# Performance work log

Measured on AMD Instinct MI355X. Metric: run time of the kernel, lower is better.

Reference implementation:

```python
import jax, jax.numpy as jnp
import numpy as np

N = 100000
E = 1600000
D = 128


def setup_inputs() -> dict:
    key = jax.random.key(0)
    k1, k2, k3 = jax.random.split(key, 3)
    indices = jax.random.randint(k1, (2, E), 0, N, dtype=jnp.int64)
    values = jax.random.normal(k2, (E,), dtype=jnp.float32)
    b = jax.random.normal(k3, (N, D), dtype=jnp.float32)
    return {"indices": indices, "values": values, "n": N, "b": b}


def reference(indices, values, n, b):
    # Sparse COO SpMM: out[r] = sum_{e: row[e]==r} values[e] * b[col[e]]
    row, col = indices[0], indices[1]
    contrib = values[:, None] * b[col]          # [E, D] gather-multiply
    out = jax.ops.segment_sum(contrib, row, num_segments=n)  # [N, D] scatter-add
    return out
```

## Files before the change

### kernel.cpp

```cpp
#include <hip/hip_runtime.h>
#include <hip/hip_fp16.h>


#define D_DIM 128
#define RPB 64
#define RPB_SHIFT 6
#define CRB 256
#define CRB_SHIFT 8
#define MAXCB 512
#define CCAP 4608
#define MAXB 2048
#define CAP_LDS 1408
#define EPT 6
#define EPT1 8
#define CHUNK1 4096
#define EPC 4
#define EPC2 5
#define OVF_T 8192

typedef float fx4 __attribute__((ext_vector_type(4)));

__global__ __launch_bounds__(256) void convert_b_kernel(
        const float* __restrict__ b, __half* __restrict__ bh, int n8) {
    int i = blockIdx.x * blockDim.x + threadIdx.x;
    if (i >= n8) return;
    const float4* b4 = (const float4*)b;
    float4 a0 = b4[2 * i];
    float4 a1 = b4[2 * i + 1];
    union { __half2 h[4]; uint4 u; } pk;
    pk.h[0] = __floats2half2_rn(a0.x, a0.y);
    pk.h[1] = __floats2half2_rn(a0.z, a0.w);
    pk.h[2] = __floats2half2_rn(a1.x, a1.y);
    pk.h[3] = __floats2half2_rn(a1.z, a1.w);
    ((uint4*)bh)[i] = pk.u;
}

__global__ __launch_bounds__(1024) void p1_sortcoarse(
        const int* __restrict__ rows,
        const int* __restrict__ cols,
        const float* __restrict__ vals,
        int* __restrict__ coarse_cnt,
        int2* __restrict__ coarse,
        int* __restrict__ ovf_cnt,
        int* __restrict__ ovf3,
        int E, int ncb, int ccap) {
    __shared__ int hist[MAXCB];
    __shared__ int cursor[MAXCB];
    __shared__ int2 stage[CHUNK1];
    __shared__ unsigned short sbkt[CHUNK1];

    int tid = threadIdx.x;
    int start = blockIdx.x * CHUNK1;
    int end = start + CHUNK1; if (end > E) end = E;
    int n = end - start;

    for (int i = tid; i < ncb; i += 1024) hist[i] = 0;
    __syncthreads();

    int rr[EPC]; int cc[EPC]; float vv[EPC];
    int ne = 0;
    for (int e = start + tid; e < end; e += 1024) {
        int r = rows[e];
        if (ne < EPC) { rr[ne] = r; cc[ne] = cols[e]; vv[ne] = vals[e]; }
        ++ne;
        atomicAdd(&hist[r >> CRB_SHIFT], 1);
    }
    __syncthreads();

    for (int d = 1; d < ncb; d <<= 1) {
        int t = (tid < ncb && tid >= d) ? hist[tid - d] : 0;
        __syncthreads();
        if (tid < ncb && tid >= d) hist[tid] += t;
        __syncthreads();
    }

    int incl = 0, excl = 0;
    if (tid < ncb) { incl = hist[tid]; excl = tid ? hist[tid - 1] : 0; }
    __syncthreads();
    if (tid < ncb) {
        int cnt = incl - excl;
        cursor[tid] = excl;
        int gres = (cnt > 0) ? atomicAdd(&coarse_cnt[tid], cnt) : 0;
        hist[tid] = gres - excl;
    }
    __syncthreads();

    for (int j = 0; j < ne; ++j) {
        int r, c; float v;
        if (j < EPC) { r = rr[j]; c = cc[j]; v = vv[j]; }
        else { int e = start + tid + j * 1024; r = rows[e]; c = cols[e]; v = vals[e]; }
        int bkt = r >> CRB_SHIFT;
        int pos = atomicAdd(&cursor[bkt], 1);
        stage[pos] = make_int2(((r & (CRB - 1)) << 17) | c, __float_as_int(v));
        sbkt[pos] = (unsigned short)bkt;
    }
    __syncthreads();

    for (int i = tid; i < n; i += 1024) {
        int bkt = sbkt[i];
        int2 e = stage[i];
        int gidx = i + hist[bkt];
        if (gidx < ccap) {
            coarse[(size_t)bkt * ccap + gidx] = e;
        } else {
            int k = atomicAdd(ovf_cnt, 1);
            if (k < OVF_T) {
                int r = (bkt << CRB_SHIFT) | ((unsigned)e.x >> 17);
                ovf3[3 * k] = r; ovf3[3 * k + 1] = e.x & 0x1FFFF;
                ovf3[3 * k + 2] = e.y;
            }
        }
    }
}

__global__ __launch_bounds__(1024) void p2_rowsort(
        const int* __restrict__ coarse_cnt,
        int2* __restrict__ coarse,
        int* __restrict__ row_beg,
        int* __restrict__ row_num,
        int ccap, int N) {
    __shared__ int2 stage[CCAP];
    __shared__ int hist[CRB];
    __shared__ int offs[CRB + 1];
    __shared__ int cursor[CRB];

    int bin = blockIdx.x;
    int tid = threadIdx.x;
    int cnt = coarse_cnt[bin];
    if (cnt > ccap) cnt = ccap;
    int2* cb = coarse + (size_t)bin * ccap;

    if (tid < CRB) hist[tid] = 0;
    __syncthreads();

    int2 ev[EPC2];
    int  rl[EPC2];
    int ne = 0;
    for (int i = tid; i < cnt; i += 1024) {
        int2 e = cb[i];
        ev[ne] = e;
        rl[ne] = ((unsigned)e.x) >> 17;
        atomicAdd(&hist[rl[ne]], 1);
        ++ne;
    }
    __syncthreads();

    for (int d = 1; d < CRB; d <<= 1) {
        int t = (tid < CRB && tid >= d) ? hist[tid - d] : 0;
        __syncthreads();
        if (tid < CRB) hist[tid] += (tid >= d) ? t : 0;
        __syncthreads();
    }
    if (tid == 0) offs[0] = 0;
    if (tid < CRB) {
        offs[tid + 1] = hist[tid];
        cursor[tid] = (tid == 0) ? 0 : hist[tid - 1];
    }
    __syncthreads();

    for (int j = 0; j < ne; ++j) {
        int pos = atomicAdd(&cursor[rl[j]], 1);
        stage[pos] = make_int2(ev[j].x & 0x1FFFF, ev[j].y);
    }
    __syncthreads();

    for (int i = tid; i < cnt; i += 1024) cb[i] = stage[i];
    if (tid < CRB) {
        int r = (bin << CRB_SHIFT) + tid;
        if (r < N) {
            row_beg[r] = bin * ccap + offs[tid];
            row_num[r] = offs[tid + 1] - offs[tid];
        }
    }
}

template <bool HALF>
__global__ __launch_bounds__(256) void csr_gather(
        const int* __restrict__ row_beg,
        const int* __restrict__ row_num,
        const int2* __restrict__ csr,
        const __half* __restrict__ bh,
        const float* __restrict__ b,
        float* __restrict__ out,
        int N) {
    int g = threadIdx.x >> 5;
    int glane = threadIdx.x & 31;
    int r = blockIdx.x * 8 + g;
    if (r >= N) return;

    int beg = row_beg[r];
    int num = row_num[r];
    const int2* pk = csr + beg;

    float4 acc = make_float4(0.f, 0.f, 0.f, 0.f);
    for (int base = 0; base < num; base += 8) {
#pragma unroll
        for (int j = 0; j < 8; ++j) {
            int idx = base + j;
            int sidx = (idx < num) ? idx : (num - 1);
            int2 e = pk[sidx];
            float v = (idx < num) ? __int_as_float(e.y) : 0.f;
            if (HALF) {
                uint2 hv = ((const uint2*)(bh + (size_t)e.x * D_DIM))[glane];
                __half2* hp = (__half2*)&hv;
                float2 f0 = __half22float2(hp[0]);
                float2 f1 = __half22float2(hp[1]);
                acc.x += v * f0.x;
                acc.y += v * f0.y;
                acc.z += v * f1.x;
                acc.w += v * f1.y;
            } else {
                float4 bv = ((const float4*)(b + (size_t)e.x * D_DIM))[glane];
                acc.x += v * bv.x;
                acc.y += v * bv.y;
                acc.z += v * bv.z;
                acc.w += v * bv.w;
            }
        }
    }
    fx4 av = {acc.x, acc.y, acc.z, acc.w};
    __builtin_nontemporal_store(av, (fx4*)(out + (size_t)r * D_DIM) + glane);
}


__global__ __launch_bounds__(1024) void phase1_partition(
        const int* __restrict__ rows,
        const int* __restrict__ cols,
        const float* __restrict__ vals,
        int* __restrict__ bucket_cnt,
        int2* __restrict__ packed,
        int* __restrict__ ovf_cnt,
        int* __restrict__ ovf3,
        int E, int nb, int cap, int chunk) {
    __shared__ int hist[MAXB];
    int tid = threadIdx.x;
    int start = blockIdx.x * chunk;
    int end = start + chunk; if (end > E) end = E;

    for (int i = tid; i < nb; i += 1024) hist[i] = 0;
    __syncthreads();

    int rr[EPT1]; int cc[EPT1]; float vv[EPT1];
    int ne = 0;
    for (int e = start + tid; e < end; e += 1024) {
        int r = rows[e];
        if (ne < EPT1) { rr[ne] = r; cc[ne] = cols[e]; vv[ne] = vals[e]; }
        ++ne;
        atomicAdd(&hist[r >> RPB_SHIFT], 1);
    }
    __syncthreads();

    for (int bkt = tid; bkt < nb; bkt += 1024) {
        int c = hist[bkt];
        hist[bkt] = (c > 0) ? atomicAdd(&bucket_cnt[bkt], c) : 0;
    }
    __syncthreads();

    int j = 0;
    for (int e = start + tid; e < end; e += 1024, ++j) {
        int r, c; float v;
        if (j < EPT1) { r = rr[j]; c = cc[j]; v = vv[j]; }
        else          { r = rows[e]; c = cols[e]; v = vals[e]; }
        int bkt = r >> RPB_SHIFT;
        int local = atomicAdd(&hist[bkt], 1);
        if (local < cap) {
            int key = ((r & (RPB - 1)) << 17) | c;
            packed[(size_t)bkt * cap + local] = make_int2(key, __float_as_int(v));
        } else {
            int k = atomicAdd(ovf_cnt, 1);
            if (k < OVF_T) {
                ovf3[3 * k] = r; ovf3[3 * k + 1] = c;
                ovf3[3 * k + 2] = __float_as_int(v);
            }
        }
    }
}

template <bool HALF>
__global__ __launch_bounds__(256) void phase2_sort_gather(
        const int* __restrict__ bucket_cnt,
        const int2* __restrict__ packed,
        const __half* __restrict__ bh,
        const float* __restrict__ b,
        float* __restrict__ out,
        int cap, int N) {
    __shared__ int2 sorted[CAP_LDS];
    __shared__ int hist[RPB];
    __shared__ int offs[RPB + 1];
    __shared__ int cursor[RPB];

    int bucket = blockIdx.x;
    int tid = threadIdx.x;

    int cnt = bucket_cnt[bucket];
    if (cnt > cap) cnt = cap;
    const int2* pk = packed + (size_t)bucket * cap;

    if (tid < RPB) hist[tid] = 0;
    __syncthreads();

    int2 ev[EPT];
    int  rl[EPT];
    int ne = 0;
    for (int i = tid; i < cnt; i += 256) {
        int2 e = pk[i];
        ev[ne] = e;
        rl[ne] = ((unsigned)e.x) >> 17;
        atomicAdd(&hist[rl[ne]], 1);
        ++ne;
    }
    __syncthreads();

    for (int d = 1; d < RPB; d <<= 1) {
        int t = (tid < RPB && tid >= d) ? hist[tid - d] : 0;
        __syncthreads();
        if (tid < RPB) hist[tid] += t;
        __syncthreads();
    }
    if (tid == 0) offs[0] = 0;
    if (tid < RPB) {
        offs[tid + 1] = hist[tid];
        cursor[tid] = (tid == 0) ? 0 : hist[tid - 1];
    }
    __syncthreads();

    for (int j = 0; j < ne; ++j) {
        int pos = atomicAdd(&cursor[rl[j]], 1);
        sorted[pos] = make_int2(ev[j].x & 0x1FFFF, ev[j].y);
    }
    __syncthreads();

    int g = tid >> 5;
    int glane = tid & 31;
    int r0 = bucket << RPB_SHIFT;
    for (int k = 0; k < 8; ++k) {
        int rr = g * 8 + k;
        int start = offs[rr];
        int num = offs[rr + 1] - start;
        float4 acc = make_float4(0.f, 0.f, 0.f, 0.f);
        for (int base = 0; base < num; base += 8) {
#pragma unroll
            for (int j = 0; j < 8; ++j) {
                int idx = base + j;
                int sidx = start + ((idx < num) ? idx : (num - 1));
                int2 e = sorted[sidx];
                float v = (idx < num) ? __int_as_float(e.y) : 0.f;
                if (HALF) {
                    uint2 hv = ((const uint2*)(bh + (size_t)e.x * D_DIM))[glane];
                    __half2* hp = (__half2*)&hv;
                    float2 f0 = __half22float2(hp[0]);
                    float2 f1 = __half22float2(hp[1]);
                    acc.x += v * f0.x;
                    acc.y += v * f0.y;
                    acc.z += v * f1.x;
                    acc.w += v * f1.y;
                } else {
                    float4 bv = ((const float4*)(b + (size_t)e.x * D_DIM))[glane];
                    acc.x += v * bv.x;
                    acc.y += v * bv.y;
                    acc.z += v * bv.z;
                    acc.w += v * bv.w;
                }
            }
        }
        int r = r0 + rr;
        if (r < N) {
            fx4 av = {acc.x, acc.y, acc.z, acc.w};
            __builtin_nontemporal_store(av, (fx4*)(out + (size_t)r * D_DIM) + glane);
        }
    }
}

__global__ void fixup_kernel(const int* __restrict__ ovf_cnt,
                             const int* __restrict__ ovf3,
                             const float* __restrict__ b,
                             float* __restrict__ out) {
    int items = *ovf_cnt;
    if (items > OVF_T) items = OVF_T;
    int gsz  = (gridDim.x * blockDim.x) >> 5;
    int gid  = (blockIdx.x * blockDim.x + threadIdx.x) >> 5;
    int lane = threadIdx.x & 31;
    for (int i = gid; i < items; i += gsz) {
        int r = ovf3[3 * i];
        int c = ovf3[3 * i + 1];
        float v = __int_as_float(ovf3[3 * i + 2]);
        float4 bv = ((const float4*)(b + (size_t)c * D_DIM))[lane];
        float* op = out + (size_t)r * D_DIM + (size_t)lane * 4;
        atomicAdd(op + 0, v * bv.x);
        atomicAdd(op + 1, v * bv.y);
        atomicAdd(op + 2, v * bv.z);
        atomicAdd(op + 3, v * bv.w);
    }
}

__global__ void spmm_atomic_kernel(const int* __restrict__ rows,
                                   const int* __restrict__ cols,
                                   const float* __restrict__ vals,
                                   const float* __restrict__ b,
                                   float* __restrict__ out, int E) {
    int t = blockIdx.x * blockDim.x + threadIdx.x;
    int e = t >> 5;
    if (e >= E) return;
    int lane = t & 31;
    int r = rows[e];
    int c = cols[e];
    float v = vals[e];
    float4 bv = ((const float4*)(b + (size_t)c * D_DIM))[lane];
    float* op = out + (size_t)r * D_DIM + (size_t)lane * 4;
    atomicAdd(op + 0, v * bv.x);
    atomicAdd(op + 1, v * bv.y);
    atomicAdd(op + 2, v * bv.z);
    atomicAdd(op + 3, v * bv.w);
}

extern "C" void kernel_launch(void* const* d_in, const int* in_sizes, int n_in,
                              void* d_out, int out_size, void* d_ws, size_t ws_size,
                              hipStream_t stream) {
    const int*   indices = (const int*)d_in[0];
    const float* vals    = (const float*)d_in[1];
    const float* b       = (const float*)d_in[3];
    float*       out     = (float*)d_out;

    int E = in_sizes[1];
    int N = out_size / D_DIM;
    const int* rows = indices;
    const int* cols = indices + E;

    int nb  = (N + RPB - 1) >> RPB_SHIFT;
    int ncb = (N + CRB - 1) >> CRB_SHIFT;
    int avg  = (nb  > 0) ? E / nb  : 0;
    int cavg = (ncb > 0) ? E / ncb : 0;
    size_t bh_bytes = (size_t)N * D_DIM * 2;
    int n8 = N * D_DIM / 8;

    {
        bool ok = (ncb <= MAXCB) && (N <= 131072) && (cavg + cavg / 8 <= CCAP);
        size_t rb_off = (size_t)ncb * 4;
        size_t rn_off = rb_off + (size_t)N * 4;
        size_t oc_off = rn_off + (size_t)N * 4;
        size_t o3_off = oc_off + 4;
        size_t co_off = (o3_off + (size_t)OVF_T * 12 + 255) & ~(size_t)255;
        size_t bh_off = (co_off + (size_t)ncb * CCAP * 8 + 255) & ~(size_t)255;
        if (ok && ws_size >= bh_off + bh_bytes) {
            char* w = (char*)d_ws;
            int*    coarse_cnt = (int*)w;
            int*    row_beg    = (int*)(w + rb_off);
            int*    row_num    = (int*)(w + rn_off);
            int*    ovf_cnt    = (int*)(w + oc_off);
            int*    ovf3       = (int*)(w + o3_off);
            int2*   coarse     = (int2*)(w + co_off);
            __half* bh         = (__half*)(w + bh_off);

            (void)hipMemsetAsync(coarse_cnt, 0, (size_t)ncb * 4, stream);
            (void)hipMemsetAsync(ovf_cnt, 0, 4, stream);

            int nwg1 = (E + CHUNK1 - 1) / CHUNK1;
            p1_sortcoarse<<<nwg1, 1024, 0, stream>>>(
                rows, cols, vals, coarse_cnt, coarse, ovf_cnt, ovf3,
                E, ncb, CCAP);

            p2_rowsort<<<ncb, 1024, 0, stream>>>(
                coarse_cnt, coarse, row_beg, row_num, CCAP, N);

            convert_b_kernel<<<(n8 + 255) / 256, 256, 0, stream>>>(b, bh, n8);

            csr_gather<true><<<(N + 7) / 8, 256, 0, stream>>>(
                row_beg, row_num, coarse, bh, b, out, N);

            fixup_kernel<<<8, 256, 0, stream>>>(ovf_cnt, ovf3, b, out);
            return;
        }
    }

    int cap = CAP_LDS;
    size_t fixed      = (size_t)nb * 4 + 4 + (size_t)OVF_T * 12;
    size_t bh_off     = (fixed + 255) & ~(size_t)255;
    size_t packed_h   = (bh_off + bh_bytes + 255) & ~(size_t)255;
    size_t packed_f   = bh_off;
    size_t need_h     = packed_h + (size_t)nb * cap * 8;
    size_t need_f     = packed_f + (size_t)nb * cap * 8;

    bool okBase = (nb <= MAXB) && (N <= 131072) && (cap > avg + avg / 8);
    bool useHalf = okBase && (ws_size >= need_h);
    bool useF32  = okBase && !useHalf && (ws_size >= need_f);

    if (!useHalf && !useF32) {
        (void)hipMemsetAsync(d_out, 0, (size_t)out_size * sizeof(float), stream);
        long long total = (long long)E * 32;
        int blocks = (int)((total + 255) / 256);
        spmm_atomic_kernel<<<blocks, 256, 0, stream>>>(rows, cols, vals, b, out, E);
        return;
    }

    char* w = (char*)d_ws;
    int*    bucket_cnt = (int*)w;
    int*    ovf_cnt    = (int*)(w + (size_t)nb * 4);
    int*    ovf3       = (int*)(w + (size_t)nb * 4 + 4);
    __half* bh         = (__half*)(w + bh_off);
    int2*   packed     = (int2*)(w + (useHalf ? packed_h : packed_f));

    (void)hipMemsetAsync(bucket_cnt, 0, (size_t)nb * 4 + 4, stream);

    if (useHalf)
        convert_b_kernel<<<(n8 + 255) / 256, 256, 0, stream>>>(b, bh, n8);

    const int P1_WGS = 256;
    int chunk = (E + P1_WGS - 1) / P1_WGS;
    phase1_partition<<<P1_WGS, 1024, 0, stream>>>(
        rows, cols, vals, bucket_cnt, packed, ovf_cnt, ovf3, E, nb, cap, chunk);

    if (useHalf)
        phase2_sort_gather<true><<<nb, 256, 0, stream>>>(
            bucket_cnt, packed, bh, b, out, cap, N);
    else
        phase2_sort_gather<false><<<nb, 256, 0, stream>>>(
            bucket_cnt, packed, bh, b, out, cap, N);

    fixup_kernel<<<8, 256, 0, stream>>>(ovf_cnt, ovf3, b, out);
}
```

Measured before the change: 232.9 us.

## Fuse row sort and CSR gather into one kernel using LDS-staged edges

The per-bin row sort and the gather-multiply are merged into a single kernel. Each block now reads its row-sorted edges straight from shared memory instead of writing them back to global memory and re-reading them through row_beg/row_num arrays. The two memsets are merged into one, and the fp16 conversion of b is launched before partitioning. This removes a kernel launch and a global round trip of the edge list. The cost is that the gather now runs on only one block per 256 rows, with each 32-lane group walking 8 rows in sequence, so there is less parallelism and more load imbalance across CUs.

```diff
diff --git a/kernel.cpp b/kernel.cpp
--- a/kernel.cpp
+++ b/kernel.cpp
@@ -113,11 +113,11 @@
     }
 }
 
-__global__ __launch_bounds__(1024) void p2_rowsort(
+__global__ __launch_bounds__(1024) void p2_sortgather(
         const int* __restrict__ coarse_cnt,
-        int2* __restrict__ coarse,
-        int* __restrict__ row_beg,
-        int* __restrict__ row_num,
+        const int2* __restrict__ coarse,
+        const __half* __restrict__ bh,
+        float* __restrict__ out,
         int ccap, int N) {
     __shared__ int2 stage[CCAP];
     __shared__ int hist[CRB];
@@ -128,7 +128,7 @@
     int tid = threadIdx.x;
     int cnt = coarse_cnt[bin];
     if (cnt > ccap) cnt = ccap;
-    int2* cb = coarse + (size_t)bin * ccap;
+    const int2* cb = coarse + (size_t)bin * ccap;
 
     if (tid < CRB) hist[tid] = 0;
     __syncthreads();
@@ -164,43 +164,21 @@
     }
     __syncthreads();
 
-    for (int i = tid; i < cnt; i += 1024) cb[i] = stage[i];
-    if (tid < CRB) {
-        int r = (bin << CRB_SHIFT) + tid;
-        if (r < N) {
-            row_beg[r] = bin * ccap + offs[tid];
-            row_num[r] = offs[tid + 1] - offs[tid];
-        }
-    }
-}
-
-template <bool HALF>
-__global__ __launch_bounds__(256) void csr_gather(
-        const int* __restrict__ row_beg,
-        const int* __restrict__ row_num,
-        const int2* __restrict__ csr,
-        const __half* __restrict__ bh,
-        const float* __restrict__ b,
-        float* __restrict__ out,
-        int N) {
-    int g = threadIdx.x >> 5;
-    int glane = threadIdx.x & 31;
-    int r = blockIdx.x * 8 + g;
-    if (r >= N) return;
-
-    int beg = row_beg[r];
-    int num = row_num[r];
-    const int2* pk = csr + beg;
-
-    float4 acc = make_float4(0.f, 0.f, 0.f, 0.f);
-    for (int base = 0; base < num; base += 8) {
+    int g = tid >> 5;
+    int glane = tid & 31;
+    int r0 = bin << CRB_SHIFT;
+    for (int k = 0; k < 8; ++k) {
+        int rr = g * 8 + k;
+        int start = offs[rr];
+        int num = offs[rr + 1] - start;
+        float4 acc = make_float4(0.f, 0.f, 0.f, 0.f);
+        for (int base = 0; base < num; base += 8) {
 #pragma unroll
-        for (int j = 0; j < 8; ++j) {
-            int idx = base + j;
-            int sidx = (idx < num) ? idx : (num - 1);
-            int2 e = pk[sidx];
-            float v = (idx < num) ? __int_as_float(e.y) : 0.f;
-            if (HALF) {
+            for (int j = 0; j < 8; ++j) {
+                int idx = base + j;
+                int sidx = start + ((idx < num) ? idx : (num - 1));
+                int2 e = stage[sidx];
+                float v = (idx < num) ? __int_as_float(e.y) : 0.f;
                 uint2 hv = ((const uint2*)(bh + (size_t)e.x * D_DIM))[glane];
                 __half2* hp = (__half2*)&hv;
                 float2 f0 = __half22float2(hp[0]);
@@ -209,17 +187,14 @@
                 acc.y += v * f0.y;
                 acc.z += v * f1.x;
                 acc.w += v * f1.y;
-            } else {
-                float4 bv = ((const float4*)(b + (size_t)e.x * D_DIM))[glane];
-                acc.x += v * bv.x;
-                acc.y += v * bv.y;
-                acc.z += v * bv.z;
-                acc.w += v * bv.w;
             }
         }
-    }
-    fx4 av = {acc.x, acc.y, acc.z, acc.w};
-    __builtin_nontemporal_store(av, (fx4*)(out + (size_t)r * D_DIM) + glane);
+        int r = r0 + rr;
+        if (r < N) {
+            fx4 av = {acc.x, acc.y, acc.z, acc.w};
+            __builtin_nontemporal_store(av, (fx4*)(out + (size_t)r * D_DIM) + glane);
+        }
+    }
 }
 
 
@@ -435,37 +410,29 @@
 
     {
         bool ok = (ncb <= MAXCB) && (N <= 131072) && (cavg + cavg / 8 <= CCAP);
-        size_t rb_off = (size_t)ncb * 4;
-        size_t rn_off = rb_off + (size_t)N * 4;
-        size_t oc_off = rn_off + (size_t)N * 4;
+        size_t oc_off = (size_t)ncb * 4;
         size_t o3_off = oc_off + 4;
         size_t co_off = (o3_off + (size_t)OVF_T * 12 + 255) & ~(size_t)255;
         size_t bh_off = (co_off + (size_t)ncb * CCAP * 8 + 255) & ~(size_t)255;
         if (ok && ws_size >= bh_off + bh_bytes) {
             char* w = (char*)d_ws;
             int*    coarse_cnt = (int*)w;
-            int*    row_beg    = (int*)(w + rb_off);
-            int*    row_num    = (int*)(w + rn_off);
             int*    ovf_cnt    = (int*)(w + oc_off);
             int*    ovf3       = (int*)(w + o3_off);
             int2*   coarse     = (int2*)(w + co_off);
             __half* bh         = (__half*)(w + bh_off);
 
-            (void)hipMemsetAsync(coarse_cnt, 0, (size_t)ncb * 4, stream);
-            (void)hipMemsetAsync(ovf_cnt, 0, 4, stream);
+            (void)hipMemsetAsync(coarse_cnt, 0, (size_t)ncb * 4 + 4, stream);
+
+            convert_b_kernel<<<(n8 + 255) / 256, 256, 0, stream>>>(b, bh, n8);
 
             int nwg1 = (E + CHUNK1 - 1) / CHUNK1;
             p1_sortcoarse<<<nwg1, 1024, 0, stream>>>(
                 rows, cols, vals, coarse_cnt, coarse, ovf_cnt, ovf3,
                 E, ncb, CCAP);
 
-            p2_rowsort<<<ncb, 1024, 0, stream>>>(
-                coarse_cnt, coarse, row_beg, row_num, CCAP, N);
-
-            convert_b_kernel<<<(n8 + 255) / 256, 256, 0, stream>>>(b, bh, n8);
-
-            csr_gather<true><<<(N + 7) / 8, 256, 0, stream>>>(
-                row_beg, row_num, coarse, bh, b, out, N);
+            p2_sortgather<<<ncb, 1024, 0, stream>>>(
+                coarse_cnt, coarse, bh, out, CCAP, N);
 
             fixup_kernel<<<8, 256, 0, stream>>>(ovf_cnt, ovf3, b, out);
             return;
```

Result: faster. 206.9 us (-11.2%).
